# Optimization experiments

Measured on AMD Instinct MI355X. Metric: run time of the kernel, lower is better.

The kernel has to match this reference:

```python
import jax, jax.numpy as jnp
import numpy as np

FEAT = 512
COND = 768
N_HEADS = 8
D_HEAD = 64
D_ATTN = N_HEADS * D_HEAD  # 512


def setup_inputs() -> dict:
    key = jax.random.key(0)
    ks = jax.random.split(key, 8)
    B, N, M = 16, 4096, 77
    x = jax.random.normal(ks[0], (B, N, FEAT), dtype=jnp.float32)
    cond = jax.random.normal(ks[1], (B, M, COND), dtype=jnp.float32)
    s_f = 1.0 / np.sqrt(FEAT)
    s_c = 1.0 / np.sqrt(COND)
    s_a = 1.0 / np.sqrt(D_ATTN)
    Wq = jax.random.normal(ks[2], (FEAT, D_ATTN), dtype=jnp.float32) * s_f
    Wk = jax.random.normal(ks[3], (COND, D_ATTN), dtype=jnp.float32) * s_c
    Wv = jax.random.normal(ks[4], (COND, D_ATTN), dtype=jnp.float32) * s_c
    Wo = jax.random.normal(ks[5], (D_ATTN, FEAT), dtype=jnp.float32) * s_a
    bo = jax.random.normal(ks[6], (FEAT,), dtype=jnp.float32) * 0.01
    return {"x": x, "cond": cond, "Wq": Wq, "Wk": Wk, "Wv": Wv, "Wo": Wo, "bo": bo}


def reference(x, cond, Wq, Wk, Wv, Wo, bo):
    B, N, _ = x.shape
    M = cond.shape[1]
    scale = D_HEAD ** (-0.5)
    # projections (no bias, as in nn.Linear(..., bias=False))
    q = (x @ Wq).reshape(B, N, N_HEADS, D_HEAD)
    k = (cond @ Wk).reshape(B, M, N_HEADS, D_HEAD)
    v = (cond @ Wv).reshape(B, M, N_HEADS, D_HEAD)
    attn = jnp.einsum('bihd,bjhd->bhij', q, k) * scale  # [B,H,N,M]
    attn = jax.nn.softmax(attn, axis=-1)  # split-half inplace softmax == plain softmax
    out = jnp.einsum('bhij,bjhd->bihd', attn, v).reshape(B, N, D_ATTN)
    return out @ Wo + bo
```

## Files before the change

kernel.cpp:

```cpp
#include <hip/hip_runtime.h>

typedef __attribute__((ext_vector_type(8))) _Float16 f16x8;
typedef __attribute__((ext_vector_type(4))) float f32x4;

#define B_SZ   16
#define N_SEQ  4096
#define M_CTX  77
#define M_PAD  96
#define NH     8

__device__ __forceinline__ _Float16 f2h(float x) { return (_Float16)x; }

__device__ __forceinline__ void gload16(const void* g, void* l) {
    __builtin_amdgcn_global_load_lds(
        (const __attribute__((address_space(1))) unsigned int*)g,
        (__attribute__((address_space(3))) unsigned int*)l, 16, 0, 0);
}

template<int C>
__device__ __forceinline__ float dppf(float x) {
    union { float f; int i; } u, v;
    u.f = x;
    v.i = __builtin_amdgcn_mov_dpp(u.i, C, 0xF, 0xF, true);
    return v.f;
}
__device__ __forceinline__ float rmax16(float x) {
    x = fmaxf(x, dppf<0xB1>(x));
    x = fmaxf(x, dppf<0x4E>(x));
    x = fmaxf(x, dppf<0x141>(x));
    x = fmaxf(x, dppf<0x140>(x));
    return x;
}
__device__ __forceinline__ float rsum16(float x) {
    x += dppf<0xB1>(x);
    x += dppf<0x4E>(x);
    x += dppf<0x141>(x);
    x += dppf<0x140>(x);
    return x;
}

__global__ __launch_bounds__(256)
void convert(const float4* __restrict__ x, f16x8* __restrict__ xh, int n8)
{
    int idx = blockIdx.x * 256 + threadIdx.x;
    int stride = gridDim.x * 256;
    for (int i = idx; i < n8; i += stride) {
        float4 a = x[2 * i];
        float4 b = x[2 * i + 1];
        f16x8 o;
        o[0] = f2h(a.x); o[1] = f2h(a.y); o[2] = f2h(a.z); o[3] = f2h(a.w);
        o[4] = f2h(b.x); o[5] = f2h(b.y); o[6] = f2h(b.z); o[7] = f2h(b.w);
        xh[i] = o;
    }
}

__global__ __launch_bounds__(256)
void prep(const float* __restrict__ Wq, const float* __restrict__ Wk,
          const float* __restrict__ Wv, const float* __restrict__ Wo,
          _Float16* __restrict__ WqT, _Float16* __restrict__ WkT,
          _Float16* __restrict__ WvT, _Float16* __restrict__ WoT)
{
    __shared__ float t[32][33];
    const float* W; _Float16* WT; int K; float scale = 1.0f;
    switch (blockIdx.z) {
        case 0:  W = Wq; WT = WqT; K = 512; scale = 0.125f; break;
        case 1:  W = Wk; WT = WkT; K = 768; break;
        case 2:  W = Wv; WT = WvT; K = 768; break;
        default: W = Wo; WT = WoT; K = 512; break;
    }
    const int ky = blockIdx.y;
    if (ky * 32 >= K) return;
    const int nx = blockIdx.x;
    const int tr = threadIdx.x >> 5, tc = threadIdx.x & 31;
#pragma unroll
    for (int i = 0; i < 4; ++i) {
        int kr = tr + i * 8;
        t[kr][tc] = W[(size_t)(ky * 32 + kr) * 512 + nx * 32 + tc];
    }
    __syncthreads();
#pragma unroll
    for (int i = 0; i < 4; ++i) {
        int nr = tr + i * 8;
        WT[(size_t)(nx * 32 + nr) * K + ky * 32 + tc] = f2h(t[tc][nr] * scale);
    }
}

__global__ __launch_bounds__(256)
void kv_proj(const float* __restrict__ cond, const _Float16* __restrict__ WkT,
             const _Float16* __restrict__ WvT, _Float16* __restrict__ Kswz,
             _Float16* __restrict__ Vswz)
{
    const int tid = threadIdx.x;
    const int l = tid & 63, w = tid >> 6;
    const int lrow = l & 15, lk = l >> 4;
    const int h = blockIdx.x, b = blockIdx.y, which = blockIdx.z;
    const _Float16* WT = which ? WvT : WkT;
    const float* cb = cond + (size_t)b * M_CTX * 768;

    f32x4 acc[5];
#pragma unroll
    for (int i = 0; i < 5; ++i)
#pragma unroll
        for (int e = 0; e < 4; ++e) acc[i][e] = 0.f;

    const int n = h * 64 + w * 16 + lrow;
    for (int kk = 0; kk < 24; ++kk) {
        f16x8 bfrag = *(const f16x8*)(WT + (size_t)n * 768 + kk * 32 + lk * 8);
#pragma unroll
        for (int rt = 0; rt < 5; ++rt) {
            int m = rt * 16 + lrow;
            f16x8 afrag;
#pragma unroll
            for (int j = 0; j < 8; ++j) afrag[j] = (_Float16)0.f;
            if (m < M_CTX) {
                const float* a = cb + (size_t)m * 768 + kk * 32 + lk * 8;
                float4 f0 = *(const float4*)a;
                float4 f1 = *(const float4*)(a + 4);
                afrag[0] = f2h(f0.x); afrag[1] = f2h(f0.y);
                afrag[2] = f2h(f0.z); afrag[3] = f2h(f0.w);
                afrag[4] = f2h(f1.x); afrag[5] = f2h(f1.y);
                afrag[6] = f2h(f1.z); afrag[7] = f2h(f1.w);
            }
            acc[rt] = __builtin_amdgcn_mfma_f32_16x16x32_f16(afrag, bfrag, acc[rt], 0, 0, 0);
        }
    }

    const int bh = b * NH + h;
    const int d = w * 16 + lrow;
    const int dhi = d >> 3, dlo = d & 7;
    if (which == 0) {
        _Float16* Kb = Kswz + (size_t)bh * (M_PAD * 64);
#pragma unroll
        for (int rt = 0; rt < 5; ++rt)
#pragma unroll
            for (int r = 0; r < 4; ++r) {
                int m = rt * 16 + lk * 4 + r;
                Kb[m * 64 + ((dhi ^ (m & 7)) * 8) + dlo] = f2h(acc[rt][r]);
            }
#pragma unroll
        for (int r = 0; r < 4; ++r) {
            int m = 80 + lk * 4 + r;
            Kb[m * 64 + ((dhi ^ (m & 7)) * 8) + dlo] = (_Float16)0.f;
        }
    } else {
        _Float16* Vb = Vswz + (size_t)bh * (64 * 128);
#pragma unroll
        for (int rt = 0; rt < 5; ++rt)
#pragma unroll
            for (int r = 0; r < 4; ++r) {
                int m = rt * 16 + lk * 4 + r;
                Vb[d * 128 + (((m >> 3) ^ dlo) * 8) + (m & 7)] = f2h(acc[rt][r]);
            }
#pragma unroll
        for (int r = 0; r < 4; ++r) {
            int m = 80 + lk * 4 + r;
            Vb[d * 128 + (((m >> 3) ^ dlo) * 8) + (m & 7)] = (_Float16)0.f;
        }
    }
}

template<int EMODE>
__global__ __launch_bounds__(256)
void gemm512(const _Float16* __restrict__ A, const _Float16* __restrict__ BT,
             void* __restrict__ Cv, const float* __restrict__ bias)
{
    __shared__ _Float16 As[128 * 64];
    __shared__ _Float16 Bs[128 * 64];

    const int bid = blockIdx.x;
    const int wg = (bid & 7) * 256 + (bid >> 3);
    const int rb = wg >> 2;
    const int cb = wg & 3;
    const size_t row0 = (size_t)rb * 128;
    const int col0 = cb * 128;

    const int tid = threadIdx.x;
    const int l = tid & 63;
    const int w = tid >> 6;
    const int wy = w >> 1, wx = w & 1;
    const int lrow = l & 15, lk = l >> 4;

    f32x4 acc[4][4];
#pragma unroll
    for (int i = 0; i < 4; ++i)
#pragma unroll
        for (int j = 0; j < 4; ++j)
#pragma unroll
            for (int e = 0; e < 4; ++e) acc[i][j][e] = 0.f;

    const int srow_in_seg = l >> 3;
    const int sslot = (l & 7) ^ (srow_in_seg & 7);
    const _Float16* a_src0 = A + (row0 + (size_t)(w * 32 + srow_in_seg)) * 512 + sslot * 8;
    const _Float16* b_src0 = BT + ((size_t)(col0 + w * 32 + srow_in_seg)) * 512 + sslot * 8;

    for (int kt = 0; kt < 8; ++kt) {
        const _Float16* ak = a_src0 + kt * 64;
        const _Float16* bk = b_src0 + kt * 64;
#pragma unroll
        for (int s = 0; s < 4; ++s) {
            gload16(ak + (size_t)s * 8 * 512, As + (w * 4 + s) * 512);
            gload16(bk + (size_t)s * 8 * 512, Bs + (w * 4 + s) * 512);
        }
        __syncthreads();

#pragma unroll
        for (int kk = 0; kk < 2; ++kk) {
            f16x8 af[4], bf[4];
#pragma unroll
            for (int mt = 0; mt < 4; ++mt) {
                int R = wy * 64 + mt * 16 + lrow;
                int p = (kk * 4 + lk) ^ (lrow & 7);
                af[mt] = *(const f16x8*)&As[R * 64 + p * 8];
            }
#pragma unroll
            for (int nt = 0; nt < 4; ++nt) {
                int R = wx * 64 + nt * 16 + lrow;
                int p = (kk * 4 + lk) ^ (lrow & 7);
                bf[nt] = *(const f16x8*)&Bs[R * 64 + p * 8];
            }
#pragma unroll
            for (int mt = 0; mt < 4; ++mt)
#pragma unroll
                for (int nt = 0; nt < 4; ++nt)
                    acc[mt][nt] = __builtin_amdgcn_mfma_f32_16x16x32_f16(af[mt], bf[nt], acc[mt][nt], 0, 0, 0);
        }
        __syncthreads();
    }

#pragma unroll
    for (int mt = 0; mt < 4; ++mt)
#pragma unroll
        for (int nt = 0; nt < 4; ++nt)
#pragma unroll
            for (int r = 0; r < 4; ++r) {
                size_t row = row0 + wy * 64 + mt * 16 + lk * 4 + r;
                int col = col0 + wx * 64 + nt * 16 + lrow;
                float v = acc[mt][nt][r];
                if (EMODE == 0) {
                    ((_Float16*)Cv)[row * 512 + col] = f2h(v);
                } else {
                    ((float*)Cv)[row * 512 + col] = v + bias[col];
                }
            }
}

__global__ __launch_bounds__(256)
void attn(const _Float16* __restrict__ Q, const _Float16* __restrict__ Kswz,
          const _Float16* __restrict__ Vswz, _Float16* __restrict__ AO)
{
    __shared__ _Float16 Ks[M_PAD * 64];
    __shared__ _Float16 Vs[64 * 128];
    __shared__ _Float16 Pl[4][16][104];

    const int tid = threadIdx.x;
    const int l = tid & 63, w = tid >> 6;
    const int lrow = l & 15, lk = l >> 4;
    const int chunk = blockIdx.x, h = blockIdx.y, b = blockIdx.z;
    const int bh = b * NH + h;

    {
        const _Float16* Kg = Kswz + (size_t)bh * (M_PAD * 64);
        const _Float16* Vg = Vswz + (size_t)bh * (64 * 128);
#pragma unroll
        for (int i = 0; i < 3; ++i) {
            int c = w * 3 + i;
            gload16(Kg + c * 512 + l * 8, Ks + c * 512);
        }
#pragma unroll
        for (int i = 0; i < 4; ++i) {
            int c = w * 4 + i;
            gload16(Vg + c * 512 + l * 8, Vs + c * 512);
        }
    }

    const size_t row0 = (size_t)b * N_SEQ + chunk * 256 + w * 64;
    f16x8 af[4][2];
    {
        const _Float16* Qb = Q + (row0 + lrow) * 512 + h * 64 + lk * 8;
#pragma unroll
        for (int mt = 0; mt < 4; ++mt)
#pragma unroll
            for (int kk = 0; kk < 2; ++kk)
                af[mt][kk] = *(const f16x8*)(Qb + (size_t)mt * 16 * 512 + kk * 32);
    }

    for (int idx = l; idx < 256; idx += 64)
        Pl[w][idx >> 4][80 + (idx & 15)] = (_Float16)0.f;

    __syncthreads();

    const bool m4ok = (lrow < 13);
    const int kswz = lrow & 7;

#pragma unroll
    for (int mt = 0; mt < 4; ++mt) {
        f32x4 s[5];
#pragma unroll
        for (int i = 0; i < 5; ++i)
#pragma unroll
            for (int e = 0; e < 4; ++e) s[i][e] = 0.f;
#pragma unroll
        for (int kk = 0; kk < 2; ++kk)
#pragma unroll
            for (int ct = 0; ct < 5; ++ct) {
                f16x8 kf = *(const f16x8*)&Ks[(ct * 16 + lrow) * 64 + (((kk * 4 + lk) ^ kswz) * 8)];
                s[ct] = __builtin_amdgcn_mfma_f32_16x16x32_f16(af[mt][kk], kf, s[ct], 0, 0, 0);
            }

        float rinv[4];
#pragma unroll
        for (int r = 0; r < 4; ++r) {
            float v0 = s[0][r], v1 = s[1][r], v2 = s[2][r], v3 = s[3][r], v4 = s[4][r];
            float mx = fmaxf(fmaxf(v0, v1), fmaxf(v2, v3));
            mx = fmaxf(mx, m4ok ? v4 : -1e30f);
            mx = rmax16(mx);
            float e0 = __expf(v0 - mx), e1 = __expf(v1 - mx);
            float e2 = __expf(v2 - mx), e3 = __expf(v3 - mx);
            float e4 = m4ok ? __expf(v4 - mx) : 0.f;
            float sum = ((e0 + e1) + (e2 + e3)) + e4;
            sum = rsum16(sum);
            rinv[r] = 1.0f / sum;
            int prow = lk * 4 + r;
            Pl[w][prow][lrow]      = f2h(e0);
            Pl[w][prow][16 + lrow] = f2h(e1);
            Pl[w][prow][32 + lrow] = f2h(e2);
            Pl[w][prow][48 + lrow] = f2h(e3);
            Pl[w][prow][64 + lrow] = f2h(e4);
        }

        f32x4 o[4];
#pragma unroll
        for (int i = 0; i < 4; ++i)
#pragma unroll
            for (int e2 = 0; e2 < 4; ++e2) o[i][e2] = 0.f;
#pragma unroll
        for (int kk = 0; kk < 3; ++kk) {
            f16x8 pa = *(const f16x8*)&Pl[w][lrow][kk * 32 + lk * 8];
#pragma unroll
            for (int ctd = 0; ctd < 4; ++ctd) {
                f16x8 vf = *(const f16x8*)&Vs[(ctd * 16 + lrow) * 128 + (((kk * 4 + lk) ^ kswz) * 8)];
                o[ctd] = __builtin_amdgcn_mfma_f32_16x16x32_f16(pa, vf, o[ctd], 0, 0, 0);
            }
        }

        const size_t rw = row0 + mt * 16 + lk * 4;
#pragma unroll
        for (int ctd = 0; ctd < 4; ++ctd)
#pragma unroll
            for (int r = 0; r < 4; ++r)
                AO[(rw + r) * 512 + h * 64 + ctd * 16 + lrow] = f2h(o[ctd][r] * rinv[r]);
    }
}

extern "C" void kernel_launch(void* const* d_in, const int* in_sizes, int n_in,
                              void* d_out, int out_size, void* d_ws, size_t ws_size,
                              hipStream_t stream)
{
    (void)in_sizes; (void)n_in; (void)out_size; (void)ws_size;
    const float* x    = (const float*)d_in[0];
    const float* cond = (const float*)d_in[1];
    const float* Wq   = (const float*)d_in[2];
    const float* Wk   = (const float*)d_in[3];
    const float* Wv   = (const float*)d_in[4];
    const float* Wo   = (const float*)d_in[5];
    const float* bo   = (const float*)d_in[6];

    char* ws = (char*)d_ws;
    _Float16* WqT  = (_Float16*)(ws);
    _Float16* WoT  = (_Float16*)(ws + 524288);
    _Float16* Kswz = (_Float16*)(ws + 1048576);
    _Float16* Vswz = (_Float16*)(ws + 2621440);
    _Float16* xh   = (_Float16*)(ws + 4718592);
    _Float16* WkT  = (_Float16*)(ws + 4718592);
    _Float16* WvT  = (_Float16*)(ws + 4718592 + 786432);
    _Float16* AO   = xh;
    _Float16* Qf   = (_Float16*)d_out;

    prep<<<dim3(16, 24, 4), 256, 0, stream>>>(Wq, Wk, Wv, Wo, WqT, WkT, WvT, WoT);
    kv_proj<<<dim3(8, 16, 2), 256, 0, stream>>>(cond, WkT, WvT, Kswz, Vswz);
    convert<<<dim3(2048), 256, 0, stream>>>((const float4*)x, (f16x8*)xh, 16 * 4096 * 512 / 8);
    gemm512<0><<<dim3(2048), 256, 0, stream>>>(xh, WqT, Qf, nullptr);
    attn<<<dim3(16, 8, 16), 256, 0, stream>>>(Qf, Kswz, Vswz, AO);
    gemm512<1><<<dim3(2048), 256, 0, stream>>>(AO, WoT, d_out, bo);
}
```

Measured before the change: 228.1 us.

## Fuse fp32-to-fp16 conversion into Q projection with full-K skinny GEMM tiles

Removes the separate convert kernel and folds the fp32→fp16 cast of x into the Q-projection GEMM, which now stages a full 64x512 A tile in LDS once. Both 512-wide GEMMs are restructured so each 512-thread block computes a full 64-row by 512-column output strip, with B fragments read straight from global memory (L2-resident weights) and no k-loop barriers. This cuts the extra read and write of x and the per-k synchronisation, but it moves B traffic into per-lane global loads with no LDS reuse and uses 64KB of LDS per block, which may lower occupancy.

```diff
diff --git a/kernel.cpp b/kernel.cpp
--- a/kernel.cpp
+++ b/kernel.cpp
@@ -37,21 +37,6 @@
     x += dppf<0x141>(x);
     x += dppf<0x140>(x);
     return x;
-}
-
-__global__ __launch_bounds__(256)
-void convert(const float4* __restrict__ x, f16x8* __restrict__ xh, int n8)
-{
-    int idx = blockIdx.x * 256 + threadIdx.x;
-    int stride = gridDim.x * 256;
-    for (int i = idx; i < n8; i += stride) {
-        float4 a = x[2 * i];
-        float4 b = x[2 * i + 1];
-        f16x8 o;
-        o[0] = f2h(a.x); o[1] = f2h(a.y); o[2] = f2h(a.z); o[3] = f2h(a.w);
-        o[4] = f2h(b.x); o[5] = f2h(b.y); o[6] = f2h(b.z); o[7] = f2h(b.w);
-        xh[i] = o;
-    }
 }
 
 __global__ __launch_bounds__(256)
@@ -159,27 +144,46 @@
     }
 }
 
-template<int EMODE>
-__global__ __launch_bounds__(256)
-void gemm512(const _Float16* __restrict__ A, const _Float16* __restrict__ BT,
-             void* __restrict__ Cv, const float* __restrict__ bias)
-{
-    __shared__ _Float16 As[128 * 64];
-    __shared__ _Float16 Bs[128 * 64];
+template<int QMODE>
+__global__ __launch_bounds__(512)
+void gemm_skinny(const void* __restrict__ Av, const _Float16* __restrict__ BT,
+                 void* __restrict__ Cv, const float* __restrict__ bias)
+{
+    __shared__ _Float16 As[64 * 512];
 
     const int bid = blockIdx.x;
-    const int wg = (bid & 7) * 256 + (bid >> 3);
-    const int rb = wg >> 2;
-    const int cb = wg & 3;
-    const size_t row0 = (size_t)rb * 128;
-    const int col0 = cb * 128;
+    const int wg = (bid & 7) * 128 + (bid >> 3);
+    const size_t row0 = (size_t)wg * 64;
 
     const int tid = threadIdx.x;
-    const int l = tid & 63;
-    const int w = tid >> 6;
-    const int wy = w >> 1, wx = w & 1;
+    const int l = tid & 63, w = tid >> 6;
     const int lrow = l & 15, lk = l >> 4;
 
+    if (QMODE) {
+        const float* X = (const float*)Av;
+        const int row = tid >> 3;
+        const int sb = tid & 7;
+        const float* src = X + (row0 + row) * 512 + sb * 8;
+        _Float16* dst = As + row * 512;
+#pragma unroll
+        for (int i = 0; i < 8; ++i) {
+            float4 f0 = *(const float4*)(src + i * 64);
+            float4 f1 = *(const float4*)(src + i * 64 + 4);
+            f16x8 v;
+            v[0] = f2h(f0.x); v[1] = f2h(f0.y); v[2] = f2h(f0.z); v[3] = f2h(f0.w);
+            v[4] = f2h(f1.x); v[5] = f2h(f1.y); v[6] = f2h(f1.z); v[7] = f2h(f1.w);
+            *(f16x8*)&dst[(((i * 8 + sb) ^ (row & 7)) * 8)] = v;
+        }
+    } else {
+        const _Float16* A = (const _Float16*)Av;
+#pragma unroll
+        for (int i = 0; i < 8; ++i) {
+            const int row = w * 8 + i;
+            gload16(A + (row0 + row) * 512 + ((l ^ (row & 7)) * 8), As + row * 512);
+        }
+    }
+    __syncthreads();
+
     f32x4 acc[4][4];
 #pragma unroll
     for (int i = 0; i < 4; ++i)
@@ -188,43 +192,24 @@
 #pragma unroll
             for (int e = 0; e < 4; ++e) acc[i][j][e] = 0.f;
 
-    const int srow_in_seg = l >> 3;
-    const int sslot = (l & 7) ^ (srow_in_seg & 7);
-    const _Float16* a_src0 = A + (row0 + (size_t)(w * 32 + srow_in_seg)) * 512 + sslot * 8;
-    const _Float16* b_src0 = BT + ((size_t)(col0 + w * 32 + srow_in_seg)) * 512 + sslot * 8;
-
-    for (int kt = 0; kt < 8; ++kt) {
-        const _Float16* ak = a_src0 + kt * 64;
-        const _Float16* bk = b_src0 + kt * 64;
-#pragma unroll
-        for (int s = 0; s < 4; ++s) {
-            gload16(ak + (size_t)s * 8 * 512, As + (w * 4 + s) * 512);
-            gload16(bk + (size_t)s * 8 * 512, Bs + (w * 4 + s) * 512);
-        }
-        __syncthreads();
-
-#pragma unroll
-        for (int kk = 0; kk < 2; ++kk) {
-            f16x8 af[4], bf[4];
-#pragma unroll
-            for (int mt = 0; mt < 4; ++mt) {
-                int R = wy * 64 + mt * 16 + lrow;
-                int p = (kk * 4 + lk) ^ (lrow & 7);
-                af[mt] = *(const f16x8*)&As[R * 64 + p * 8];
-            }
-#pragma unroll
-            for (int nt = 0; nt < 4; ++nt) {
-                int R = wx * 64 + nt * 16 + lrow;
-                int p = (kk * 4 + lk) ^ (lrow & 7);
-                bf[nt] = *(const f16x8*)&Bs[R * 64 + p * 8];
-            }
-#pragma unroll
-            for (int mt = 0; mt < 4; ++mt)
-#pragma unroll
-                for (int nt = 0; nt < 4; ++nt)
-                    acc[mt][nt] = __builtin_amdgcn_mfma_f32_16x16x32_f16(af[mt], bf[nt], acc[mt][nt], 0, 0, 0);
-        }
-        __syncthreads();
+    const _Float16* Ab = As + lrow * 512;
+    const int sxor = lrow & 7;
+    const _Float16* bb = BT + (size_t)(w * 64 + lrow) * 512 + lk * 8;
+
+#pragma unroll 2
+    for (int kt = 0; kt < 16; ++kt) {
+        f16x8 af[4], bf[4];
+#pragma unroll
+        for (int nt = 0; nt < 4; ++nt)
+            bf[nt] = *(const f16x8*)(bb + (size_t)nt * 16 * 512 + kt * 32);
+#pragma unroll
+        for (int mt = 0; mt < 4; ++mt)
+            af[mt] = *(const f16x8*)(Ab + mt * 16 * 512 + (((kt * 4 + lk) ^ sxor) * 8));
+#pragma unroll
+        for (int mt = 0; mt < 4; ++mt)
+#pragma unroll
+            for (int nt = 0; nt < 4; ++nt)
+                acc[mt][nt] = __builtin_amdgcn_mfma_f32_16x16x32_f16(af[mt], bf[nt], acc[mt][nt], 0, 0, 0);
     }
 
 #pragma unroll
@@ -233,10 +218,10 @@
         for (int nt = 0; nt < 4; ++nt)
 #pragma unroll
             for (int r = 0; r < 4; ++r) {
-                size_t row = row0 + wy * 64 + mt * 16 + lk * 4 + r;
-                int col = col0 + wx * 64 + nt * 16 + lrow;
+                size_t row = row0 + mt * 16 + lk * 4 + r;
+                int col = w * 64 + nt * 16 + lrow;
                 float v = acc[mt][nt][r];
-                if (EMODE == 0) {
+                if (QMODE) {
                     ((_Float16*)Cv)[row * 512 + col] = f2h(v);
                 } else {
                     ((float*)Cv)[row * 512 + col] = v + bias[col];
@@ -370,16 +355,14 @@
     _Float16* WoT  = (_Float16*)(ws + 524288);
     _Float16* Kswz = (_Float16*)(ws + 1048576);
     _Float16* Vswz = (_Float16*)(ws + 2621440);
-    _Float16* xh   = (_Float16*)(ws + 4718592);
+    _Float16* AO   = (_Float16*)(ws + 4718592);
     _Float16* WkT  = (_Float16*)(ws + 4718592);
     _Float16* WvT  = (_Float16*)(ws + 4718592 + 786432);
-    _Float16* AO   = xh;
     _Float16* Qf   = (_Float16*)d_out;
 
     prep<<<dim3(16, 24, 4), 256, 0, stream>>>(Wq, Wk, Wv, Wo, WqT, WkT, WvT, WoT);
     kv_proj<<<dim3(8, 16, 2), 256, 0, stream>>>(cond, WkT, WvT, Kswz, Vswz);
-    convert<<<dim3(2048), 256, 0, stream>>>((const float4*)x, (f16x8*)xh, 16 * 4096 * 512 / 8);
-    gemm512<0><<<dim3(2048), 256, 0, stream>>>(xh, WqT, Qf, nullptr);
+    gemm_skinny<1><<<dim3(1024), 512, 0, stream>>>(x, WqT, Qf, nullptr);
     attn<<<dim3(16, 8, 16), 256, 0, stream>>>(Qf, Kswz, Vswz, AO);
-    gemm512<1><<<dim3(2048), 256, 0, stream>>>(AO, WoT, d_out, bo);
-}
+    gemm_skinny<0><<<dim3(1024), 512, 0, stream>>>(AO, WoT, (float*)d_out, bo);
+}
```

After: 249.2 us. +9.2%, slower.

## Double-buffer LDS tiles in projection GEMMs to overlap loads with MFMA

Applied to the files above, without the earlier changes.

Both projection GEMMs now use two LDS buffers per operand. The next K-tile is loaded with global_load_lds while MFMAs run on the current tile, using one waitcnt and barrier per iteration instead of two syncthreads. MFMA sections are also wrapped in s_setprio. This doubles LDS use to 64KB per block, which may lower occupancy, and the vmcnt(0) wait still blocks on the prefetch before each iteration starts.

```diff
diff --git a/kernel.cpp b/kernel.cpp
--- a/kernel.cpp
+++ b/kernel.cpp
@@ -16,6 +16,9 @@
         (const __attribute__((address_space(1))) unsigned int*)g,
         (__attribute__((address_space(3))) unsigned int*)l, 16, 0, 0);
 }
+
+#define BAR()    asm volatile("s_barrier" ::: "memory")
+#define WAITV0() asm volatile("s_waitcnt vmcnt(0)" ::: "memory")
 
 template<int C>
 __device__ __forceinline__ float dppf(float x) {
@@ -161,11 +164,11 @@
 
 template<int EMODE>
 __global__ __launch_bounds__(256)
-void gemm512(const _Float16* __restrict__ A, const _Float16* __restrict__ BT,
+void gemm_db(const _Float16* __restrict__ A, const _Float16* __restrict__ BT,
              void* __restrict__ Cv, const float* __restrict__ bias)
 {
-    __shared__ _Float16 As[128 * 64];
-    __shared__ _Float16 Bs[128 * 64];
+    __shared__ _Float16 As[2][128 * 64];
+    __shared__ _Float16 Bs[2][128 * 64];
 
     const int bid = blockIdx.x;
     const int wg = (bid & 7) * 256 + (bid >> 3);
@@ -188,20 +191,29 @@
 #pragma unroll
             for (int e = 0; e < 4; ++e) acc[i][j][e] = 0.f;
 
-    const int srow_in_seg = l >> 3;
-    const int sslot = (l & 7) ^ (srow_in_seg & 7);
-    const _Float16* a_src0 = A + (row0 + (size_t)(w * 32 + srow_in_seg)) * 512 + sslot * 8;
-    const _Float16* b_src0 = BT + ((size_t)(col0 + w * 32 + srow_in_seg)) * 512 + sslot * 8;
-
-    for (int kt = 0; kt < 8; ++kt) {
+    const int srow = l >> 3;
+    const int sslot = (l & 7) ^ (srow & 7);
+    const _Float16* a_src0 = A + (row0 + (size_t)(w * 32 + srow)) * 512 + sslot * 8;
+    const _Float16* b_src0 = BT + ((size_t)(col0 + w * 32 + srow)) * 512 + sslot * 8;
+
+    auto stage = [&](int kt) {
+        const int buf = kt & 1;
         const _Float16* ak = a_src0 + kt * 64;
         const _Float16* bk = b_src0 + kt * 64;
 #pragma unroll
         for (int s = 0; s < 4; ++s) {
-            gload16(ak + (size_t)s * 8 * 512, As + (w * 4 + s) * 512);
-            gload16(bk + (size_t)s * 8 * 512, Bs + (w * 4 + s) * 512);
-        }
-        __syncthreads();
+            gload16(ak + (size_t)s * 8 * 512, &As[buf][(w * 4 + s) * 512]);
+            gload16(bk + (size_t)s * 8 * 512, &Bs[buf][(w * 4 + s) * 512]);
+        }
+    };
+
+    stage(0);
+
+    for (int kt = 0; kt < 8; ++kt) {
+        const int buf = kt & 1;
+        WAITV0();
+        BAR();
+        if (kt < 7) stage(kt + 1);
 
 #pragma unroll
         for (int kk = 0; kk < 2; ++kk) {
@@ -210,21 +222,22 @@
             for (int mt = 0; mt < 4; ++mt) {
                 int R = wy * 64 + mt * 16 + lrow;
                 int p = (kk * 4 + lk) ^ (lrow & 7);
-                af[mt] = *(const f16x8*)&As[R * 64 + p * 8];
+                af[mt] = *(const f16x8*)&As[buf][R * 64 + p * 8];
             }
 #pragma unroll
             for (int nt = 0; nt < 4; ++nt) {
                 int R = wx * 64 + nt * 16 + lrow;
                 int p = (kk * 4 + lk) ^ (lrow & 7);
-                bf[nt] = *(const f16x8*)&Bs[R * 64 + p * 8];
-            }
+                bf[nt] = *(const f16x8*)&Bs[buf][R * 64 + p * 8];
+            }
+            __builtin_amdgcn_s_setprio(1);
 #pragma unroll
             for (int mt = 0; mt < 4; ++mt)
 #pragma unroll
                 for (int nt = 0; nt < 4; ++nt)
                     acc[mt][nt] = __builtin_amdgcn_mfma_f32_16x16x32_f16(af[mt], bf[nt], acc[mt][nt], 0, 0, 0);
-        }
-        __syncthreads();
+            __builtin_amdgcn_s_setprio(0);
+        }
     }
 
 #pragma unroll
@@ -379,7 +392,7 @@
     prep<<<dim3(16, 24, 4), 256, 0, stream>>>(Wq, Wk, Wv, Wo, WqT, WkT, WvT, WoT);
     kv_proj<<<dim3(8, 16, 2), 256, 0, stream>>>(cond, WkT, WvT, Kswz, Vswz);
     convert<<<dim3(2048), 256, 0, stream>>>((const float4*)x, (f16x8*)xh, 16 * 4096 * 512 / 8);
-    gemm512<0><<<dim3(2048), 256, 0, stream>>>(xh, WqT, Qf, nullptr);
+    gemm_db<0><<<dim3(2048), 256, 0, stream>>>(xh, WqT, Qf, nullptr);
     attn<<<dim3(16, 8, 16), 256, 0, stream>>>(Qf, Kswz, Vswz, AO);
-    gemm512<1><<<dim3(2048), 256, 0, stream>>>(AO, WoT, d_out, bo);
-}
+    gemm_db<1><<<dim3(2048), 256, 0, stream>>>(AO, WoT, d_out, bo);
+}
```

After: 220.1 us. -3.5%, faster.
